# Kernel tuning notes

Hardware: AMD Instinct MI355X
Metric: run time of the kernel (lower is better)

## Reference

```python
import jax, jax.numpy as jnp
import numpy as np
from jax import lax

T = 8192
D_MODEL = 768
D_RNN = 1024
KW = 4  # conv kernel width


def setup_inputs() -> dict:
    key = jax.random.key(0)
    ks = jax.random.split(key, 9)
    x = jax.random.normal(ks[0], (T, D_MODEL), jnp.float32)
    # equinox nn.Linear(in, out): weight [out, in], bias [out]
    w1 = jax.random.normal(ks[1], (2 * D_RNN, D_MODEL), jnp.float32) / np.sqrt(D_MODEL)
    b1 = jnp.zeros((2 * D_RNN,), jnp.float32)
    # nn.Conv1d(d_rnn, d_rnn, 4, use_bias=False): kernel [out_ch, in_ch, kw]
    conv_w = jax.random.normal(ks[2], (D_RNN, D_RNN, KW), jnp.float32) / np.sqrt(D_RNN * KW)
    w_rg = jax.random.normal(ks[3], (2 * D_RNN, D_RNN), jnp.float32) / np.sqrt(D_RNN)
    b_rg = jnp.zeros((2 * D_RNN,), jnp.float32)
    w_out = jax.random.normal(ks[4], (D_MODEL, D_RNN), jnp.float32) / np.sqrt(D_RNN)
    b_out = jnp.zeros((D_MODEL,), jnp.float32)
    # Lambda ~ U(inv_sigmoid(0.9)^{1/8}, inv_sigmoid(0.999)^{1/8}) as in __init__
    inv_sig = lambda p: np.log(1.0 / (1.0 - p))
    lower = np.power(inv_sig(0.9), 1.0 / 8.0)
    upper = np.power(inv_sig(0.999), 1.0 / 8.0)
    Lambda = jax.random.uniform(ks[5], (D_RNN,), jnp.float32, lower, upper)
    return {"x": x, "w1": w1, "b1": b1, "conv_w": conv_w, "w_rg": w_rg,
            "b_rg": b_rg, "w_out": w_out, "b_out": b_out, "Lambda": Lambda}


def _rglru_forward(x, w1, b1, conv_w, w_rg, b_rg, w_out, b_out, Lambda):
    # lin1 then split into gate branch (gelu) and recurrent branch
    h = x @ w1.T + b1                       # [T, 2*D_RNN]
    a_branch = jax.nn.gelu(h[:, :D_RNN])    # [T, D_RNN]
    b_branch = h[:, D_RNN:]                 # [T, D_RNN]
    # causal conv1d: lhs [N=1, C, T], rhs [O, I, KW], left pad 3
    bc = lax.conv_general_dilated(b_branch.T[None], conv_w, (1,), [(KW - 1, 0)])[0].T  # [T, D_RNN]
    # RG-LRU gating
    g = jax.nn.sigmoid(bc @ w_rg.T + b_rg)  # [T, 2*D_RNN]
    inp_gate = g[:, :D_RNN]
    rec_gate = g[:, D_RNN:]
    a_t = jnp.exp(-8.0 * jax.nn.softplus(Lambda)[None, :] * rec_gate)  # [T, D_RNN]
    gated_x = jnp.sqrt(1.0 - a_t ** 2) * inp_gate * bc

    def rec_step(state, xs):
        gx, av = xs
        hn = av * state + gx
        return hn, hn

    _, y = lax.scan(rec_step, jnp.zeros((D_RNN,), x.dtype), (gated_x, a_t))
    return (a_branch * y) @ w_out.T + b_out  # [T, D_MODEL]


def reference(x, w1, b1, conv_w, w_rg, b_rg, w_out, b_out, Lambda):
    return _rglru_forward(x, w1, b1, conv_w, w_rg, b_rg, w_out, b_out, Lambda)
```

## Files before the change

### kernel.cpp

```cpp
#include <hip/hip_runtime.h>
#include <hip/hip_bf16.h>
#include <stdint.h>


#define T_LEN 8192
#define DM 768
#define DR 1024
#define NC 128
#define CL 64

typedef __bf16 bf16x8 __attribute__((ext_vector_type(8)));
typedef float  f32x4  __attribute__((ext_vector_type(4)));

#define AS1 __attribute__((address_space(1)))
#define AS3 __attribute__((address_space(3)))

__device__ __forceinline__ void cp16_g2l(const void* g, void* l) {
    __builtin_amdgcn_global_load_lds((const AS1 void*)g, (AS3 void*)l, 16, 0, 0);
}

__device__ __forceinline__ float gelu_tanh(float x) {
    const float inner = 0.7978845608028654f * (x + 0.044715f * x * x * x);
    return 0.5f * x * (1.f + tanhf(inner));
}

__device__ __forceinline__ __bf16 f2b(float v) {
    __hip_bfloat16 h = __float2bfloat16(v);
    return *reinterpret_cast<__bf16*>(&h);
}

template<int BN, int EPI, bool SHIFT>
__global__ __launch_bounds__(256, 4)
void gemm_mfma(const __hip_bfloat16* __restrict__ A,
               const __hip_bfloat16* __restrict__ B,
               const float* __restrict__ bias,
               void* __restrict__ Cv,
               int K, int lda, int N,
               __hip_bfloat16* __restrict__ D2)
{
    constexpr int NI  = BN / 32;
    constexpr int BLD = (BN * 4) / 256;
    constexpr int NLD = 2 + BLD;
    __shared__ __align__(16) unsigned char smem[32768];
    __bf16* Asb = (__bf16*)smem;
    __bf16* Bsb = (__bf16*)(smem + 16384);

    const int tid  = threadIdx.x;
    const int lane = tid & 63;
    const int wave = tid >> 6;
    const size_t m0 = (size_t)blockIdx.x * 128;
    const int    n0 = blockIdx.y * BN;
    const int wm = (wave >> 1) * 64;
    const int wn = (wave & 1) * (BN / 2);

    f32x4 acc[4][NI];
#pragma unroll
    for (int i = 0; i < 4; ++i)
#pragma unroll
        for (int j = 0; j < NI; ++j)
            acc[i][j] = f32x4{0.f, 0.f, 0.f, 0.f};

    const int frow = lane & 15;
    const int fq   = lane >> 4;

    auto stage = [&](int buf, int k0) {
#pragma unroll
        for (int q = 0; q < 2; ++q) {
            const int lin = q * 256 + tid;
            const int rr  = lin >> 2;
            const int gc  = (lin & 3) ^ ((rr >> 1) & 3);
            const size_t ar = m0 + rr + (SHIFT ? (size_t)(k0 >> 10) : 0);
            const int    ac = SHIFT ? (k0 & 1023) : k0;
            cp16_g2l(A + ar * (size_t)lda + ac + gc * 8, Asb + buf * 4096 + lin * 8);
        }
#pragma unroll
        for (int q = 0; q < BLD; ++q) {
            const int lin = q * 256 + tid;
            const int rr  = lin >> 2;
            const int gc  = (lin & 3) ^ ((rr >> 1) & 3);
            cp16_g2l(B + (size_t)(n0 + rr) * K + k0 + gc * 8,
                     Bsb + buf * (BN * 32) + lin * 8);
        }
    };

    const int nt = K / 32;
    stage(0, 0);
    int cur = 0;
    for (int t = 0; t < nt; ++t) {
        if (t + 1 < nt) {
            stage(cur ^ 1, (t + 1) * 32);
            asm volatile("s_waitcnt vmcnt(%0)" :: "n"(NLD) : "memory");
        } else {
            asm volatile("s_waitcnt vmcnt(0)" ::: "memory");
        }
        __builtin_amdgcn_sched_barrier(0);
        __builtin_amdgcn_s_barrier();
        __builtin_amdgcn_sched_barrier(0);

        bf16x8 af[4], bfr[NI];
#pragma unroll
        for (int mi = 0; mi < 4; ++mi) {
            const int R = wm + mi * 16 + frow;
            af[mi] = *(const bf16x8*)&Asb[cur * 4096 + R * 32 + ((fq ^ ((R >> 1) & 3)) * 8)];
        }
#pragma unroll
        for (int ni = 0; ni < NI; ++ni) {
            const int R = wn + ni * 16 + frow;
            bfr[ni] = *(const bf16x8*)&Bsb[cur * (BN * 32) + R * 32 + ((fq ^ ((R >> 1) & 3)) * 8)];
        }
        asm volatile("s_waitcnt lgkmcnt(0)" ::: "memory");
        __builtin_amdgcn_sched_barrier(0);
        __builtin_amdgcn_s_barrier();
        __builtin_amdgcn_sched_barrier(0);

        __builtin_amdgcn_s_setprio(1);
#pragma unroll
        for (int mi = 0; mi < 4; ++mi)
#pragma unroll
            for (int ni = 0; ni < NI; ++ni)
                acc[mi][ni] = __builtin_amdgcn_mfma_f32_16x16x32_bf16(
                    af[mi], bfr[ni], acc[mi][ni], 0, 0, 0);
        __builtin_amdgcn_s_setprio(0);
        cur ^= 1;
    }

    __syncthreads();
    const int er = fq * 4;
    const int ec = frow;

    if (EPI == 0) {
        float* Cl = (float*)smem;
#pragma unroll
        for (int ni = 0; ni < NI; ++ni) {
            const int cc = wn + ni * 16 + ec;
            const float bv = bias ? bias[n0 + cc] : 0.f;
#pragma unroll
            for (int mi = 0; mi < 4; ++mi)
#pragma unroll
                for (int r2 = 0; r2 < 4; ++r2) {
                    const int R = wm + mi * 16 + er + r2;
                    Cl[R * 64 + ((((cc >> 2) ^ (R & 7)) << 2) | (cc & 3))] =
                        acc[mi][ni][r2] + bv;
                }
        }
        __syncthreads();
        float* outp = (float*)Cv;
#pragma unroll
        for (int p = 0; p < 8; ++p) {
            const int R   = (tid >> 4) + p * 16;
            const int chn = tid & 15;
            const f32x4 v = *(const f32x4*)&Cl[R * 64 + ((chn ^ (R & 7)) << 2)];
            *(f32x4*)&outp[(m0 + R) * (size_t)N + n0 + chn * 4] = v;
        }
    } else {
        __bf16* Cl = (__bf16*)smem;
        const bool ahalf = (EPI == 2) && (n0 < 1024);
#pragma unroll
        for (int ni = 0; ni < NI; ++ni) {
            const int cc = wn + ni * 16 + ec;
            const float bv = bias ? bias[n0 + cc] : 0.f;
#pragma unroll
            for (int mi = 0; mi < 4; ++mi)
#pragma unroll
                for (int r2 = 0; r2 < 4; ++r2) {
                    const int R = wm + mi * 16 + er + r2;
                    float v = acc[mi][ni][r2] + bv;
                    if (EPI == 2 && ahalf) v = gelu_tanh(v);
                    Cl[R * 128 + ((((cc >> 3) ^ (R & 7)) << 3) | (cc & 7))] = f2b(v);
                }
        }
        __syncthreads();
#pragma unroll
        for (int p = 0; p < 8; ++p) {
            const int R   = (tid >> 4) + p * 16;
            const int chn = tid & 15;
            const bf16x8 v = *(const bf16x8*)&Cl[R * 128 + ((chn ^ (R & 7)) << 3)];
            if (EPI == 1) {
                *(bf16x8*)((__bf16*)Cv + (m0 + R) * (size_t)N + n0 + chn * 8) = v;
            } else if (n0 < 1024) {
                *(bf16x8*)((__bf16*)Cv + (m0 + R) * 1024 + n0 + chn * 8) = v;
            } else {
                *(bf16x8*)((__bf16*)D2 + (m0 + R + 3) * 1024 + (n0 - 1024) + chn * 8) = v;
            }
        }
    }
}

__global__ __launch_bounds__(256, 2)
void conv_mfma(const __hip_bfloat16* __restrict__ bbp,
               const __hip_bfloat16* __restrict__ WB,
               __hip_bfloat16* __restrict__ C)
{
    __shared__ __align__(16) unsigned char smem[32768];
    __bf16* Ah = (__bf16*)smem;

    const int tid  = threadIdx.x;
    const int lane = tid & 63;
    const int wave = tid >> 6;
    const size_t m0 = (size_t)blockIdx.x * 128;
    const int    n0 = blockIdx.y * 128;
    const int wm = (wave >> 1) * 64;
    const int wn = (wave & 1) * 64;

    f32x4 acc[4][4];
#pragma unroll
    for (int i = 0; i < 4; ++i)
#pragma unroll
        for (int j = 0; j < 4; ++j)
            acc[i][j] = f32x4{0.f, 0.f, 0.f, 0.f};

    const int frow = lane & 15;
    const int fq   = lane >> 4;

    const __bf16* wbase = (const __bf16*)WB +
        ((size_t)((n0 + wn) >> 4) << 16) + (lane << 3);

    auto loadB = [&](bf16x8 (&b)[4][4], int t1) {
#pragma unroll
        for (int s = 0; s < 4; ++s)
#pragma unroll
            for (int ni = 0; ni < 4; ++ni)
                b[s][ni] = *(const bf16x8*)(wbase + ((size_t)ni << 16) +
                                            t1 * 2048 + s * 512);
    };
    auto stageA = [&](int abuf, int kc) {
#pragma unroll
        for (int q = 0; q < 2; ++q) {
            const int lin = q * 256 + tid;
            const int rr  = lin >> 2;
            const int gc  = (lin & 3) ^ ((rr >> 1) & 3);
            cp16_g2l(bbp + (m0 + rr) * 1024 + kc + gc * 8, Ah + abuf * 4224 + lin * 8);
        }
        if (tid < 16) {
            const int lin = 512 + tid;
            const int rr  = lin >> 2;
            const int gc  = (lin & 3) ^ ((rr >> 1) & 3);
            cp16_g2l(bbp + (m0 + rr) * 1024 + kc + gc * 8, Ah + abuf * 4224 + lin * 8);
        }
    };

    bf16x8 bA[4][4], bB[4][4];
    stageA(0, 0);
    loadB(bA, 0);

    auto iter = [&](bf16x8 (&bCur)[4][4], bf16x8 (&bNxt)[4][4], int t) {
        if (t + 1 < 32) {
            loadB(bNxt, t + 1);
            asm volatile("s_waitcnt vmcnt(16)" ::: "memory");
        } else {
            asm volatile("s_waitcnt vmcnt(0)" ::: "memory");
        }
        __builtin_amdgcn_sched_barrier(0);
        __builtin_amdgcn_s_barrier();
        __builtin_amdgcn_sched_barrier(0);

        const int ab = (t & 1) * 4224;
        __builtin_amdgcn_s_setprio(1);
#pragma unroll
        for (int s = 0; s < 4; ++s) {
            bf16x8 af[4];
#pragma unroll
            for (int mi = 0; mi < 4; ++mi) {
                const int R = wm + mi * 16 + frow + s;
                af[mi] = *(const bf16x8*)&Ah[ab + R * 32 + ((fq ^ ((R >> 1) & 3)) * 8)];
            }
#pragma unroll
            for (int mi = 0; mi < 4; ++mi)
#pragma unroll
                for (int ni = 0; ni < 4; ++ni)
                    acc[mi][ni] = __builtin_amdgcn_mfma_f32_16x16x32_bf16(
                        af[mi], bCur[s][ni], acc[mi][ni], 0, 0, 0);
        }
        __builtin_amdgcn_s_setprio(0);
        __builtin_amdgcn_sched_barrier(0);
        __builtin_amdgcn_s_barrier();
        __builtin_amdgcn_sched_barrier(0);
        if (t + 1 < 32) stageA((t + 1) & 1, (t + 1) * 32);
    };

#pragma unroll 1
    for (int tp = 0; tp < 16; ++tp) {
        iter(bA, bB, 2 * tp);
        iter(bB, bA, 2 * tp + 1);
    }

    __syncthreads();
    const int er = fq * 4;
    const int ec = frow;
    __bf16* Cl = (__bf16*)smem;
#pragma unroll
    for (int ni = 0; ni < 4; ++ni) {
        const int cc = wn + ni * 16 + ec;
#pragma unroll
        for (int mi = 0; mi < 4; ++mi)
#pragma unroll
            for (int r2 = 0; r2 < 4; ++r2) {
                const int R = wm + mi * 16 + er + r2;
                Cl[R * 128 + ((((cc >> 3) ^ (R & 7)) << 3) | (cc & 7))] =
                    f2b(acc[mi][ni][r2]);
            }
    }
    __syncthreads();
#pragma unroll
    for (int p = 0; p < 8; ++p) {
        const int R   = (tid >> 4) + p * 16;
        const int chn = tid & 15;
        const bf16x8 v = *(const bf16x8*)&Cl[R * 128 + ((chn ^ (R & 7)) << 3)];
        *(bf16x8*)((__bf16*)C + (m0 + R) * 1024 + n0 + chn * 8) = v;
    }
}

#define PREP_X   6291456
#define PREP_W1  (PREP_X + 1572864)
#define PREP_WRG (PREP_W1 + 2097152)
#define PREP_WO  (PREP_WRG + 786432)
#define PREP_CW  (PREP_WO + 4194304)
#define PREP_TOT (PREP_CW + 3072)
__global__ void prep_kernel(const float* __restrict__ x, const float* __restrict__ w1,
                            const float* __restrict__ w_rg, const float* __restrict__ w_out,
                            const float* __restrict__ conv_w,
                            __hip_bfloat16* __restrict__ xb, __hip_bfloat16* __restrict__ w1b,
                            __hip_bfloat16* __restrict__ w_rgb, __hip_bfloat16* __restrict__ w_outb,
                            __hip_bfloat16* __restrict__ wbigb, __hip_bfloat16* __restrict__ bbp)
{
    const int idx = blockIdx.x * 256 + threadIdx.x;
    if (idx < PREP_X) {
        xb[idx] = __float2bfloat16(x[idx]);
    } else if (idx < PREP_W1) {
        const int i = idx - PREP_X;  w1b[i] = __float2bfloat16(w1[i]);
    } else if (idx < PREP_WRG) {
        const int i = idx - PREP_W1; w_rgb[i] = __float2bfloat16(w_rg[i]);
    } else if (idx < PREP_WO) {
        const int i = idx - PREP_WRG; w_outb[i] = __float2bfloat16(w_out[i]);
    } else if (idx < PREP_CW) {
        const int n    = idx - PREP_WO;
        const int nt   = n >> 16;
        const int r1   = n & 65535;
        const int kcI  = r1 >> 11;
        const int r2   = r1 & 2047;
        const int s    = r2 >> 9;
        const int r3   = r2 & 511;
        const int l    = r3 >> 3;
        const int j0   = r3 & 7;
        const int frow = l & 15, fq = l >> 4;
        const int o = nt * 16 + frow;
        const int i = kcI * 32 + fq * 8 + j0;
        wbigb[n] = __float2bfloat16(conv_w[o * 4096 + i * 4 + s]);
    } else {
        bbp[idx - PREP_CW] = __float2bfloat16(0.f);
    }
}

__global__ void scan_pass1(const __hip_bfloat16* __restrict__ gp,
                           const __hip_bfloat16* __restrict__ bc,
                           const float* __restrict__ Lambda,
                           float* __restrict__ ch, float* __restrict__ ca)
{
    const int c = blockIdx.y * 256 + threadIdx.x;
    const int j = blockIdx.x;
    const float cl = -8.f * log1pf(expf(Lambda[c]));
    float h = 0.f, ap = 1.f;
    const int t0 = j * CL;
    for (int tt = 0; tt < CL; ++tt) {
        const int t = t0 + tt;
        const long gi = (long)t * 2048 + c;
        const float ig = 1.f / (1.f + expf(-__bfloat162float(gp[gi])));
        const float rg = 1.f / (1.f + expf(-__bfloat162float(gp[gi + 1024])));
        const float a  = expf(cl * rg);
        const float gx = sqrtf(fmaxf(0.f, 1.f - a * a)) * ig *
                         __bfloat162float(bc[(long)t * 1024 + c]);
        h  = fmaf(a, h, gx);
        ap *= a;
    }
    ch[j * 1024 + c] = h;
    ca[j * 1024 + c] = ap;
}

__global__ void scan_combine(float* __restrict__ ch, const float* __restrict__ ca)
{
    const int c = blockIdx.x * 256 + threadIdx.x;
    float carry = 0.f;
    for (int j = 0; j < NC; ++j) {
        const float hj = ch[j * 1024 + c];
        const float aj = ca[j * 1024 + c];
        ch[j * 1024 + c] = carry;
        carry = fmaf(aj, carry, hj);
    }
}

__global__ void scan_pass2(const __hip_bfloat16* __restrict__ gp, const __hip_bfloat16* bc,
                           const float* __restrict__ Lambda,
                           const float* __restrict__ carry_in,
                           const __hip_bfloat16* __restrict__ ab,
                           __hip_bfloat16* zb)
{
    const int c = blockIdx.y * 256 + threadIdx.x;
    const int j = blockIdx.x;
    const float cl = -8.f * log1pf(expf(Lambda[c]));
    float h = carry_in[j * 1024 + c];
    const int t0 = j * CL;
    for (int tt = 0; tt < CL; ++tt) {
        const int t = t0 + tt;
        const long gi = (long)t * 2048 + c;
        const long bi = (long)t * 1024 + c;
        const float ig = 1.f / (1.f + expf(-__bfloat162float(gp[gi])));
        const float rg = 1.f / (1.f + expf(-__bfloat162float(gp[gi + 1024])));
        const float a  = expf(cl * rg);
        const float gx = sqrtf(fmaxf(0.f, 1.f - a * a)) * ig * __bfloat162float(bc[bi]);
        h = fmaf(a, h, gx);
        zb[bi] = __float2bfloat16(__bfloat162float(ab[bi]) * h);
    }
}

extern "C" void kernel_launch(void* const* d_in, const int* in_sizes, int n_in,
                              void* d_out, int out_size, void* d_ws, size_t ws_size,
                              hipStream_t stream)
{
    const float* x      = (const float*)d_in[0];
    const float* w1     = (const float*)d_in[1];
    const float* b1     = (const float*)d_in[2];
    const float* conv_w = (const float*)d_in[3];
    const float* w_rg   = (const float*)d_in[4];
    const float* b_rg   = (const float*)d_in[5];
    const float* w_out  = (const float*)d_in[6];
    const float* b_out  = (const float*)d_in[7];
    const float* Lambda = (const float*)d_in[8];
    float* out = (float*)d_out;
    (void)in_sizes; (void)n_in; (void)out_size; (void)ws_size;

    char* p = (char*)d_ws;
    auto alloc = [&](size_t bytes) { char* r = p; p += (bytes + 255) & ~255ULL; return r; };
    __hip_bfloat16* gpre  = (__hip_bfloat16*)alloc(8192ULL * 2048 * 2);
    __hip_bfloat16* ab    = (__hip_bfloat16*)alloc(8192ULL * 1024 * 2);
    __hip_bfloat16* bbp   = (__hip_bfloat16*)alloc(8200ULL * 1024 * 2);
    __hip_bfloat16* bcb   = (__hip_bfloat16*)alloc(8192ULL * 1024 * 2);
    __hip_bfloat16* wbigb = (__hip_bfloat16*)alloc(1024ULL * 4096 * 2);
    __hip_bfloat16* xb    = (__hip_bfloat16*)alloc(8192ULL * 768 * 2);
    __hip_bfloat16* w1b   = (__hip_bfloat16*)alloc(2048ULL * 768 * 2);
    __hip_bfloat16* w_rgb = (__hip_bfloat16*)alloc(2048ULL * 1024 * 2);
    __hip_bfloat16* w_outb= (__hip_bfloat16*)alloc(768ULL * 1024 * 2);
    float*          chv   = (float*)alloc(NC * 1024ULL * 4);
    float*          cav   = (float*)alloc(NC * 1024ULL * 4);
    __hip_bfloat16* zb    = bcb;

    prep_kernel<<<PREP_TOT / 256, 256, 0, stream>>>(x, w1, w_rg, w_out, conv_w,
                                                    xb, w1b, w_rgb, w_outb, wbigb, bbp);

    {
        dim3 grid(T_LEN / 128, 2048 / 128);
        gemm_mfma<128, 2, false><<<grid, 256, 0, stream>>>(xb, w1b, b1, ab, DM, DM, 2048, bbp);
    }

    {
        dim3 grid(T_LEN / 128, 1024 / 128);
        conv_mfma<<<grid, 256, 0, stream>>>(bbp, wbigb, bcb);
    }

    {
        dim3 grid(T_LEN / 128, 2048 / 128);
        gemm_mfma<128, 1, false><<<grid, 256, 0, stream>>>(bcb, w_rgb, b_rg, gpre, DR, DR, 2048, nullptr);
    }

    {
        dim3 gs(NC, DR / 256);
        scan_pass1<<<gs, 256, 0, stream>>>(gpre, bcb, Lambda, chv, cav);
        scan_combine<<<DR / 256, 256, 0, stream>>>(chv, cav);
        scan_pass2<<<gs, 256, 0, stream>>>(gpre, bcb, Lambda, chv, ab, zb);
    }

    {
        dim3 grid(T_LEN / 128, DM / 64);
        gemm_mfma<64, 0, false><<<grid, 256, 0, stream>>>(zb, w_outb, b_out, out, DR, DR, DM, nullptr);
    }
}
```

Before: 268.1 us.

## Load GEMM weights directly into registers from fragment-packed layout, widen K tile

The weight matrices are pre-packed in the prep kernel into MFMA fragment order, so each lane loads its B fragments straight from global memory into registers with double buffering instead of staging them through LDS. The A tile grows to a K-step of 64 with an 8-way XOR swizzle, and the loop is unrolled by two over ping-pong register buffers. This removes the LDS traffic and LDS reads for B and halves the number of barriers. In exchange it needs more registers (launch bounds drop from 4 to 2 blocks per SM), and each block rereads weights from L2 without reuse through LDS.

```diff
diff --git a/kernel.cpp b/kernel.cpp
--- a/kernel.cpp
+++ b/kernel.cpp
@@ -29,21 +29,19 @@
     return *reinterpret_cast<__bf16*>(&h);
 }
 
-template<int BN, int EPI, bool SHIFT>
-__global__ __launch_bounds__(256, 4)
+template<int BN, int EPI>
+__global__ __launch_bounds__(256, 2)
 void gemm_mfma(const __hip_bfloat16* __restrict__ A,
-               const __hip_bfloat16* __restrict__ B,
+               const __hip_bfloat16* __restrict__ WF,
                const float* __restrict__ bias,
                void* __restrict__ Cv,
                int K, int lda, int N,
                __hip_bfloat16* __restrict__ D2)
 {
-    constexpr int NI  = BN / 32;
-    constexpr int BLD = (BN * 4) / 256;
-    constexpr int NLD = 2 + BLD;
+    constexpr int NI = BN / 32;
+    constexpr int NV = 4 + 2 * NI;
     __shared__ __align__(16) unsigned char smem[32768];
     __bf16* Asb = (__bf16*)smem;
-    __bf16* Bsb = (__bf16*)(smem + 16384);
 
     const int tid  = threadIdx.x;
     const int lane = tid & 63;
@@ -62,34 +60,40 @@
 
     const int frow = lane & 15;
     const int fq   = lane >> 4;
-
-    auto stage = [&](int buf, int k0) {
-#pragma unroll
-        for (int q = 0; q < 2; ++q) {
+    const int NKT  = K >> 5;
+    const int nt   = K >> 6;
+
+    const __bf16* wbase = (const __bf16*)WF +
+        (((size_t)((n0 + wn) >> 4) * NKT) << 9) + (lane << 3);
+
+    auto loadB = [&](bf16x8 (&b)[2][NI], int t1) {
+#pragma unroll
+        for (int ks = 0; ks < 2; ++ks)
+#pragma unroll
+            for (int ni = 0; ni < NI; ++ni)
+                b[ks][ni] = *(const bf16x8*)(wbase +
+                    (((size_t)(ni * NKT + 2 * t1 + ks)) << 9));
+    };
+    auto stageA = [&](int buf, int k0) {
+#pragma unroll
+        for (int q = 0; q < 4; ++q) {
             const int lin = q * 256 + tid;
-            const int rr  = lin >> 2;
-            const int gc  = (lin & 3) ^ ((rr >> 1) & 3);
-            const size_t ar = m0 + rr + (SHIFT ? (size_t)(k0 >> 10) : 0);
-            const int    ac = SHIFT ? (k0 & 1023) : k0;
-            cp16_g2l(A + ar * (size_t)lda + ac + gc * 8, Asb + buf * 4096 + lin * 8);
-        }
-#pragma unroll
-        for (int q = 0; q < BLD; ++q) {
-            const int lin = q * 256 + tid;
-            const int rr  = lin >> 2;
-            const int gc  = (lin & 3) ^ ((rr >> 1) & 3);
-            cp16_g2l(B + (size_t)(n0 + rr) * K + k0 + gc * 8,
-                     Bsb + buf * (BN * 32) + lin * 8);
+            const int rr  = lin >> 3;
+            const int gc  = (lin & 7) ^ (rr & 7);
+            cp16_g2l(A + (m0 + rr) * (size_t)lda + k0 + gc * 8,
+                     Asb + buf * 8192 + lin * 8);
         }
     };
 
-    const int nt = K / 32;
-    stage(0, 0);
-    int cur = 0;
-    for (int t = 0; t < nt; ++t) {
+    bf16x8 bA[2][NI], bB[2][NI];
+    stageA(0, 0);
+    loadB(bA, 0);
+
+    auto iter = [&](bf16x8 (&bCur)[2][NI], bf16x8 (&bNxt)[2][NI], int t) {
         if (t + 1 < nt) {
-            stage(cur ^ 1, (t + 1) * 32);
-            asm volatile("s_waitcnt vmcnt(%0)" :: "n"(NLD) : "memory");
+            stageA((t + 1) & 1, (t + 1) * 64);
+            loadB(bNxt, t + 1);
+            asm volatile("s_waitcnt vmcnt(%0)" :: "n"(NV) : "memory");
         } else {
             asm volatile("s_waitcnt vmcnt(0)" ::: "memory");
         }
@@ -97,31 +101,34 @@
         __builtin_amdgcn_s_barrier();
         __builtin_amdgcn_sched_barrier(0);
 
-        bf16x8 af[4], bfr[NI];
-#pragma unroll
-        for (int mi = 0; mi < 4; ++mi) {
-            const int R = wm + mi * 16 + frow;
-            af[mi] = *(const bf16x8*)&Asb[cur * 4096 + R * 32 + ((fq ^ ((R >> 1) & 3)) * 8)];
-        }
-#pragma unroll
-        for (int ni = 0; ni < NI; ++ni) {
-            const int R = wn + ni * 16 + frow;
-            bfr[ni] = *(const bf16x8*)&Bsb[cur * (BN * 32) + R * 32 + ((fq ^ ((R >> 1) & 3)) * 8)];
-        }
-        asm volatile("s_waitcnt lgkmcnt(0)" ::: "memory");
+        const int ab = (t & 1) * 8192;
+        __builtin_amdgcn_s_setprio(1);
+#pragma unroll
+        for (int ks = 0; ks < 2; ++ks) {
+            bf16x8 af[4];
+#pragma unroll
+            for (int mi = 0; mi < 4; ++mi) {
+                const int R = wm + mi * 16 + frow;
+                af[mi] = *(const bf16x8*)&Asb[ab + R * 64 +
+                                              (((ks * 4 + fq) ^ (R & 7)) * 8)];
+            }
+#pragma unroll
+            for (int mi = 0; mi < 4; ++mi)
+#pragma unroll
+                for (int ni = 0; ni < NI; ++ni)
+                    acc[mi][ni] = __builtin_amdgcn_mfma_f32_16x16x32_bf16(
+                        af[mi], bCur[ks][ni], acc[mi][ni], 0, 0, 0);
+        }
+        __builtin_amdgcn_s_setprio(0);
         __builtin_amdgcn_sched_barrier(0);
         __builtin_amdgcn_s_barrier();
         __builtin_amdgcn_sched_barrier(0);
-
-        __builtin_amdgcn_s_setprio(1);
-#pragma unroll
-        for (int mi = 0; mi < 4; ++mi)
-#pragma unroll
-            for (int ni = 0; ni < NI; ++ni)
-                acc[mi][ni] = __builtin_amdgcn_mfma_f32_16x16x32_bf16(
-                    af[mi], bfr[ni], acc[mi][ni], 0, 0, 0);
-        __builtin_amdgcn_s_setprio(0);
-        cur ^= 1;
+    };
+
+#pragma unroll 1
+    for (int tp = 0; tp < nt / 2; ++tp) {
+        iter(bA, bB, 2 * tp);
+        iter(bB, bA, 2 * tp + 1);
     }
 
     __syncthreads();
@@ -319,22 +326,46 @@
 __global__ void prep_kernel(const float* __restrict__ x, const float* __restrict__ w1,
                             const float* __restrict__ w_rg, const float* __restrict__ w_out,
                             const float* __restrict__ conv_w,
-                            __hip_bfloat16* __restrict__ xb, __hip_bfloat16* __restrict__ w1b,
-                            __hip_bfloat16* __restrict__ w_rgb, __hip_bfloat16* __restrict__ w_outb,
+                            __hip_bfloat16* __restrict__ xb, __hip_bfloat16* __restrict__ w1f,
+                            __hip_bfloat16* __restrict__ w_rgf, __hip_bfloat16* __restrict__ w_outf,
                             __hip_bfloat16* __restrict__ wbigb, __hip_bfloat16* __restrict__ bbp)
 {
     const int idx = blockIdx.x * 256 + threadIdx.x;
     if (idx < PREP_X) {
         xb[idx] = __float2bfloat16(x[idx]);
     } else if (idx < PREP_W1) {
-        const int i = idx - PREP_X;  w1b[i] = __float2bfloat16(w1[i]);
+        const int i  = idx - PREP_X;
+        const int nti = i / 12288;
+        const int r  = i % 12288;
+        const int kt = r >> 9;
+        const int r2 = r & 511;
+        const int l  = r2 >> 3, j0 = r2 & 7;
+        const int row = nti * 16 + (l & 15);
+        const int col = kt * 32 + (l >> 4) * 8 + j0;
+        w1f[i] = __float2bfloat16(w1[row * 768 + col]);
     } else if (idx < PREP_WRG) {
-        const int i = idx - PREP_W1; w_rgb[i] = __float2bfloat16(w_rg[i]);
+        const int i  = idx - PREP_W1;
+        const int nti = i >> 14;
+        const int r  = i & 16383;
+        const int kt = r >> 9;
+        const int r2 = r & 511;
+        const int l  = r2 >> 3, j0 = r2 & 7;
+        const int row = nti * 16 + (l & 15);
+        const int col = kt * 32 + (l >> 4) * 8 + j0;
+        w_rgf[i] = __float2bfloat16(w_rg[row * 1024 + col]);
     } else if (idx < PREP_WO) {
-        const int i = idx - PREP_WRG; w_outb[i] = __float2bfloat16(w_out[i]);
+        const int i  = idx - PREP_WRG;
+        const int nti = i >> 14;
+        const int r  = i & 16383;
+        const int kt = r >> 9;
+        const int r2 = r & 511;
+        const int l  = r2 >> 3, j0 = r2 & 7;
+        const int row = nti * 16 + (l & 15);
+        const int col = kt * 32 + (l >> 4) * 8 + j0;
+        w_outf[i] = __float2bfloat16(w_out[row * 1024 + col]);
     } else if (idx < PREP_CW) {
         const int n    = idx - PREP_WO;
-        const int nt   = n >> 16;
+        const int nti  = n >> 16;
         const int r1   = n & 65535;
         const int kcI  = r1 >> 11;
         const int r2   = r1 & 2047;
@@ -343,7 +374,7 @@
         const int l    = r3 >> 3;
         const int j0   = r3 & 7;
         const int frow = l & 15, fq = l >> 4;
-        const int o = nt * 16 + frow;
+        const int o = nti * 16 + frow;
         const int i = kcI * 32 + fq * 8 + j0;
         wbigb[n] = __float2bfloat16(conv_w[o * 4096 + i * 4 + s]);
     } else {
@@ -436,19 +467,19 @@
     __hip_bfloat16* bcb   = (__hip_bfloat16*)alloc(8192ULL * 1024 * 2);
     __hip_bfloat16* wbigb = (__hip_bfloat16*)alloc(1024ULL * 4096 * 2);
     __hip_bfloat16* xb    = (__hip_bfloat16*)alloc(8192ULL * 768 * 2);
-    __hip_bfloat16* w1b   = (__hip_bfloat16*)alloc(2048ULL * 768 * 2);
-    __hip_bfloat16* w_rgb = (__hip_bfloat16*)alloc(2048ULL * 1024 * 2);
-    __hip_bfloat16* w_outb= (__hip_bfloat16*)alloc(768ULL * 1024 * 2);
+    __hip_bfloat16* w1f   = (__hip_bfloat16*)alloc(2048ULL * 768 * 2);
+    __hip_bfloat16* w_rgf = (__hip_bfloat16*)alloc(2048ULL * 1024 * 2);
+    __hip_bfloat16* w_outf= (__hip_bfloat16*)alloc(768ULL * 1024 * 2);
     float*          chv   = (float*)alloc(NC * 1024ULL * 4);
     float*          cav   = (float*)alloc(NC * 1024ULL * 4);
     __hip_bfloat16* zb    = bcb;
 
     prep_kernel<<<PREP_TOT / 256, 256, 0, stream>>>(x, w1, w_rg, w_out, conv_w,
-                                                    xb, w1b, w_rgb, w_outb, wbigb, bbp);
+                                                    xb, w1f, w_rgf, w_outf, wbigb, bbp);
 
     {
         dim3 grid(T_LEN / 128, 2048 / 128);
-        gemm_mfma<128, 2, false><<<grid, 256, 0, stream>>>(xb, w1b, b1, ab, DM, DM, 2048, bbp);
+        gemm_mfma<128, 2><<<grid, 256, 0, stream>>>(xb, w1f, b1, ab, DM, DM, 2048, bbp);
     }
 
     {
@@ -458,7 +489,7 @@
 
     {
         dim3 grid(T_LEN / 128, 2048 / 128);
-        gemm_mfma<128, 1, false><<<grid, 256, 0, stream>>>(bcb, w_rgb, b_rg, gpre, DR, DR, 2048, nullptr);
+        gemm_mfma<128, 1><<<grid, 256, 0, stream>>>(bcb, w_rgf, b_rg, gpre, DR, DR, 2048, nullptr);
     }
 
     {
@@ -470,6 +501,6 @@
 
     {
         dim3 grid(T_LEN / 128, DM / 64);
-        gemm_mfma<64, 0, false><<<grid, 256, 0, stream>>>(zb, w_outb, b_out, out, DR, DR, DM, nullptr);
-    }
-}
+        gemm_mfma<64, 0><<<grid, 256, 0, stream>>>(zb, w_outf, b_out, out, DR, DR, DM, nullptr);
+    }
+}
```

Result: no change. 267.6 us (-0.2%).
